# Kernel optimization log

Hardware: AMD Instinct MI355X
Metric: run time of the kernel (lower is better)

## Reference

```python
import jax, jax.numpy as jnp
import numpy as np

HIDDEN = 192
NDIM = 3
N_NODES = 262144
BATCH = 8
N_SUPER = 2048
DEG = 16
N_EDGES = BATCH * N_SUPER * DEG  # 262144
MAX_WAVELENGTH = 10000.0


def sincos_embed(coords):
    # ContinuousSincosEmbed: dim=192, ndim=3 -> 64 dims per coord (32 sin + 32 cos), no padding
    d_per = HIDDEN // NDIM  # 64
    omega = 1.0 / MAX_WAVELENGTH ** (jnp.arange(0, d_per, 2, dtype=jnp.float32) / d_per)  # [32]
    out = coords[:, :, None] * omega[None, None, :]            # [N, ndim, 32]
    emb = jnp.concatenate([jnp.sin(out), jnp.cos(out)], -1)    # [N, ndim, 64]
    return emb.reshape(coords.shape[0], HIDDEN)                # [N, 192]


def _xavier(key, fan_in, fan_out):
    bound = np.sqrt(6.0 / (fan_in + fan_out)).astype(np.float32)
    return jax.random.uniform(key, (fan_in, fan_out), jnp.float32, -bound, bound)


def setup_inputs() -> dict:
    key = jax.random.key(0)
    k = jax.random.split(key, 8)
    mesh_pos = jax.random.normal(k[0], (N_NODES, NDIM), jnp.float32)
    # edges grouped by sorted dst (segment_csr precondition); every supernode appears DEG times
    dst = jnp.repeat(jnp.arange(BATCH * N_SUPER, dtype=jnp.int32), DEG)          # [E]
    src = jax.random.randint(k[1], (N_EDGES,), 0, N_NODES, dtype=jnp.int32)      # [E]
    mesh_edges = jnp.stack([dst, src], axis=1)                                   # [E, 2]
    batch_idx = jnp.repeat(jnp.arange(BATCH, dtype=jnp.int32), N_NODES // BATCH)
    return {
        "mesh_pos": mesh_pos,
        "mesh_edges": mesh_edges,
        "batch_idx": batch_idx,
        "W1": _xavier(k[2], 2 * HIDDEN, 2 * HIDDEN), "b1": jnp.zeros((2 * HIDDEN,), jnp.float32),
        "W2": _xavier(k[3], 2 * HIDDEN, HIDDEN),     "b2": jnp.zeros((HIDDEN,), jnp.float32),
        "W3": _xavier(k[4], HIDDEN, HIDDEN),         "b3": jnp.zeros((HIDDEN,), jnp.float32),
    }


def reference(mesh_pos, mesh_edges, batch_idx, W1, b1, W2, b2, W3, b3):
    x = sincos_embed(mesh_pos)                       # [N, H]
    dst_idx = mesh_edges[:, 0]
    src_idx = mesh_edges[:, 1]
    h = jnp.concatenate([x[src_idx], x[dst_idx]], axis=1)        # [E, 2H]
    h = jax.nn.gelu(h @ W1 + b1, approximate=False)
    h = jax.nn.gelu(h @ W2 + b2, approximate=False)
    h = h @ W3 + b3                                              # [E, H]
    num_segments = BATCH * N_SUPER  # = number of unique dst by construction
    sums = jax.ops.segment_sum(h, dst_idx, num_segments=num_segments)
    counts = jax.ops.segment_sum(jnp.ones((h.shape[0],), h.dtype), dst_idx,
                                 num_segments=num_segments)
    mean = sums / jnp.maximum(counts, 1.0)[:, None]              # segment_csr mean
    return mean.reshape(BATCH, N_SUPER, HIDDEN)
```

## Files before the change

kernel.cpp:

```cpp
#include <hip/hip_runtime.h>

#define HID    192
#define HID2   384
#define NEDGES 262144
#define NSEG   16384
#define MB     64
#define NBLK   (NEDGES / MB)

#define ALD   200
#define H1LD  408
#define SMEM2 26112

typedef __bf16 bf16;
typedef __bf16 bv8 __attribute__((ext_vector_type(8)));
typedef __bf16 bv4 __attribute__((ext_vector_type(4)));
typedef float f32x4 __attribute__((ext_vector_type(4)));

__device__ __forceinline__ float gelu_fast(float x) {
    float x2 = x * x;
    float u2 = 1.5957691216057308f * x * __builtin_fmaf(0.044715f, x2, 1.0f);
    float e  = __expf(u2);
    float inv = __builtin_amdgcn_rcpf(e + 1.0f);
    return __builtin_fmaf(-x, inv, x);
}

__device__ __forceinline__ bv8 embed8(float p0, float p1, float p2, int t0) {
    const int dim   = t0 >> 6;
    const int isCos = t0 & 32;
    const int f0    = t0 & 31;
    const float pv  = (dim == 0) ? p0 : ((dim == 1) ? p1 : p2);
    float om = exp2f(-0.4152410118609203f * (float)f0);
    bv8 v;
    #pragma unroll
    for (int j = 0; j < 8; ++j) {
        const float x = pv * om;
        v[j] = (bf16)(isCos ? __cosf(x) : __sinf(x));
        om *= 0.74989420933245582f;
    }
    return v;
}

__global__ void wprep_kernel(const float* __restrict__ W1, const float* __restrict__ W2,
                             const float* __restrict__ W3,
                             bf16* __restrict__ W1T, bf16* __restrict__ W2T,
                             bf16* __restrict__ W3T) {
    __shared__ float t[32][33];
    int b = blockIdx.x;
    const float* S; bf16* D; int K, N, tk, tn;
    if (b < 144)      { S = W1; D = W1T; K = 384; N = 384; tk = (b / 12) * 32; tn = (b % 12) * 32; }
    else if (b < 216) { b -= 144; S = W2; D = W2T; K = 384; N = 192; tk = (b / 6) * 32; tn = (b % 6) * 32; }
    else              { b -= 216; S = W3; D = W3T; K = 192; N = 192; tk = (b / 6) * 32; tn = (b % 6) * 32; }
    const int c = threadIdx.x & 31, r0 = threadIdx.x >> 5;
    #pragma unroll
    for (int i = 0; i < 4; ++i)
        t[r0 + i * 8][c] = S[(size_t)(tk + r0 + i * 8) * N + tn + c];
    __syncthreads();
    #pragma unroll
    for (int i = 0; i < 4; ++i)
        D[(size_t)(tn + r0 + i * 8) * K + tk + c] = (bf16)t[c][r0 + i * 8];
}

__global__ __launch_bounds__(256, 3)
void dstc_kernel(const float* __restrict__ pos, const int* __restrict__ edges,
                 const bf16* __restrict__ W1T, bf16* __restrict__ dstC) {
    __shared__ __align__(16) bf16 smem[MB * ALD];
    const int tid = threadIdx.x, w = tid >> 6, lane = tid & 63;
    const int quad = lane >> 4, l15 = lane & 15, blk = blockIdx.x;
    {
        const int r = tid >> 2, part = tid & 3;
        const int node = edges[2 * ((blk * MB + r) * 16)];
        const float p0 = pos[node * 3 + 0], p1 = pos[node * 3 + 1], p2 = pos[node * 3 + 2];
        bf16* ldst = smem + r * ALD + part * 48;
        #pragma unroll
        for (int g = 0; g < 6; ++g)
            *reinterpret_cast<bv8*>(ldst + g * 8) = embed8(p0, p1, p2, part * 48 + g * 8);
    }
    __syncthreads();
    const f32x4 fz = {0.f, 0.f, 0.f, 0.f};
    f32x4 acc[6][4];
    #pragma unroll
    for (int mc = 0; mc < 6; ++mc)
        #pragma unroll
        for (int ne = 0; ne < 4; ++ne) acc[mc][ne] = fz;
    const bf16* wb = W1T + (size_t)(w * 96 + l15) * HID2 + 192 + quad * 8;
    const bf16* xb = smem + l15 * ALD + quad * 8;
    for (int kt = 0; kt < 6; ++kt) {
        bv8 x[4];
        #pragma unroll
        for (int ne = 0; ne < 4; ++ne)
            x[ne] = *reinterpret_cast<const bv8*>(xb + ne * 16 * ALD + kt * 32);
        #pragma unroll
        for (int mc = 0; mc < 6; ++mc) {
            bv8 a = *reinterpret_cast<const bv8*>(wb + mc * 16 * HID2 + kt * 32);
            #pragma unroll
            for (int ne = 0; ne < 4; ++ne)
                acc[mc][ne] = __builtin_amdgcn_mfma_f32_16x16x32_bf16(a, x[ne], acc[mc][ne], 0, 0, 0);
        }
    }
    #pragma unroll
    for (int mc = 0; mc < 6; ++mc)
        #pragma unroll
        for (int ne = 0; ne < 4; ++ne) {
            bv4 pk;
            #pragma unroll
            for (int r = 0; r < 4; ++r) pk[r] = (bf16)acc[mc][ne][r];
            *reinterpret_cast<bv4*>(dstC + (size_t)(blk * MB + ne * 16 + l15) * HID2
                                    + w * 96 + mc * 16 + quad * 4) = pk;
        }
}

__global__ __launch_bounds__(256, 3)
void fused_mlp_kernel(const float* __restrict__ pos, const int* __restrict__ edges,
                      const bf16* __restrict__ W1T, const float* __restrict__ b1,
                      const bf16* __restrict__ W2T, const float* __restrict__ b2,
                      const bf16* __restrict__ dstC, bf16* __restrict__ mh2) {
    __shared__ __align__(16) bf16 smem[SMEM2];
    const int tid = threadIdx.x, w = tid >> 6, lane = tid & 63;
    const int quad = lane >> 4, l15 = lane & 15, blk = blockIdx.x;

    {
        const int r = tid >> 2, part = tid & 3;
        const int node = edges[2 * (blk * MB + r) + 1];
        const float p0 = pos[node * 3 + 0], p1 = pos[node * 3 + 1], p2 = pos[node * 3 + 2];
        bf16* ldst = smem + r * ALD + part * 48;
        #pragma unroll
        for (int g = 0; g < 6; ++g)
            *reinterpret_cast<bv8*>(ldst + g * 8) = embed8(p0, p1, p2, part * 48 + g * 8);
    }
    __syncthreads();

    const f32x4 fz = {0.f, 0.f, 0.f, 0.f};

    f32x4 acc1[6][4];
    #pragma unroll
    for (int mc = 0; mc < 6; ++mc)
        #pragma unroll
        for (int ne = 0; ne < 4; ++ne) acc1[mc][ne] = fz;
    {
        const bf16* wb = W1T + (size_t)(w * 96 + l15) * HID2 + quad * 8;
        const bf16* xb = smem + l15 * ALD + quad * 8;
        for (int kt = 0; kt < 6; ++kt) {
            bv8 x[4];
            #pragma unroll
            for (int ne = 0; ne < 4; ++ne)
                x[ne] = *reinterpret_cast<const bv8*>(xb + ne * 16 * ALD + kt * 32);
            #pragma unroll
            for (int mc = 0; mc < 6; ++mc) {
                bv8 a = *reinterpret_cast<const bv8*>(wb + mc * 16 * HID2 + kt * 32);
                #pragma unroll
                for (int ne = 0; ne < 4; ++ne)
                    acc1[mc][ne] = __builtin_amdgcn_mfma_f32_16x16x32_bf16(a, x[ne], acc1[mc][ne], 0, 0, 0);
            }
        }
    }
    __syncthreads();

    {
        const int cb = w * 96 + quad * 4;
        #pragma unroll
        for (int mc = 0; mc < 6; ++mc) {
            f32x4 bia = *reinterpret_cast<const f32x4*>(b1 + cb + mc * 16);
            #pragma unroll
            for (int ne = 0; ne < 4; ++ne) {
                bv4 dc = *reinterpret_cast<const bv4*>(dstC + (size_t)(blk * 4 + ne) * HID2 + cb + mc * 16);
                bv4 o;
                #pragma unroll
                for (int r = 0; r < 4; ++r)
                    o[r] = (bf16)gelu_fast(acc1[mc][ne][r] + (float)dc[r] + bia[r]);
                *reinterpret_cast<bv4*>(smem + (ne * 16 + l15) * H1LD + cb + mc * 16) = o;
            }
        }
    }
    __syncthreads();

    f32x4 acc2[4][3];
    #pragma unroll
    for (int m = 0; m < 4; ++m)
        #pragma unroll
        for (int nc = 0; nc < 3; ++nc) acc2[m][nc] = fz;
    {
        const bf16* hb = smem + l15 * H1LD + quad * 8;
        const bf16* wb = W2T + (size_t)(w * 48 + l15) * HID2 + quad * 8;
        for (int kt = 0; kt < 12; ++kt) {
            bv8 h[4];
            #pragma unroll
            for (int m = 0; m < 4; ++m)
                h[m] = *reinterpret_cast<const bv8*>(hb + m * 16 * H1LD + kt * 32);
            #pragma unroll
            for (int nc = 0; nc < 3; ++nc) {
                bv8 b = *reinterpret_cast<const bv8*>(wb + nc * 16 * HID2 + kt * 32);
                #pragma unroll
                for (int m = 0; m < 4; ++m)
                    acc2[m][nc] = __builtin_amdgcn_mfma_f32_16x16x32_bf16(h[m], b, acc2[m][nc], 0, 0, 0);
            }
        }
    }

    #pragma unroll
    for (int nc = 0; nc < 3; ++nc) {
        const int colv = w * 48 + nc * 16 + l15;
        const float bia = b2[colv];
        #pragma unroll
        for (int m = 0; m < 4; ++m) {
            float s = gelu_fast(acc2[m][nc][0] + bia) + gelu_fast(acc2[m][nc][1] + bia)
                    + gelu_fast(acc2[m][nc][2] + bia) + gelu_fast(acc2[m][nc][3] + bia);
            s += __shfl_xor(s, 16);
            s += __shfl_xor(s, 32);
            if (quad == 0)
                mh2[(size_t)(blk * 4 + m) * HID + colv] = (bf16)(s * 0.0625f);
        }
    }
}

__global__ __launch_bounds__(256, 3)
void gemm3_kernel(const bf16* __restrict__ mh2, const bf16* __restrict__ W3T,
                  const float* __restrict__ b3, float* __restrict__ out) {
    __shared__ __align__(16) bf16 smem[128 * ALD];
    const int tid = threadIdx.x, w = tid >> 6, lane = tid & 63;
    const int quad = lane >> 4, l15 = lane & 15, blk = blockIdx.x;
    {
        const int r = tid >> 1, half = tid & 1;
        const bf16* src = mh2 + (size_t)(blk * 128 + r) * HID + half * 96;
        bf16* dst = smem + r * ALD + half * 96;
        #pragma unroll
        for (int i = 0; i < 12; ++i)
            reinterpret_cast<bv8*>(dst)[i] = reinterpret_cast<const bv8*>(src)[i];
    }
    __syncthreads();
    const f32x4 fz = {0.f, 0.f, 0.f, 0.f};
    f32x4 acc[8][3];
    #pragma unroll
    for (int mt = 0; mt < 8; ++mt)
        #pragma unroll
        for (int nc = 0; nc < 3; ++nc) acc[mt][nc] = fz;
    {
        const bf16* hb = smem + l15 * ALD + quad * 8;
        const bf16* wb = W3T + (size_t)(w * 48 + l15) * HID + quad * 8;
        for (int kt = 0; kt < 6; ++kt) {
            bv8 h[8];
            #pragma unroll
            for (int mt = 0; mt < 8; ++mt)
                h[mt] = *reinterpret_cast<const bv8*>(hb + mt * 16 * ALD + kt * 32);
            #pragma unroll
            for (int nc = 0; nc < 3; ++nc) {
                bv8 b = *reinterpret_cast<const bv8*>(wb + nc * 16 * HID + kt * 32);
                #pragma unroll
                for (int mt = 0; mt < 8; ++mt)
                    acc[mt][nc] = __builtin_amdgcn_mfma_f32_16x16x32_bf16(h[mt], b, acc[mt][nc], 0, 0, 0);
            }
        }
    }
    #pragma unroll
    for (int nc = 0; nc < 3; ++nc) {
        const int col = w * 48 + nc * 16 + l15;
        const float bia = b3[col];
        #pragma unroll
        for (int mt = 0; mt < 8; ++mt)
            #pragma unroll
            for (int r = 0; r < 4; ++r)
                out[(size_t)(blk * 128 + mt * 16 + quad * 4 + r) * HID + col] = acc[mt][nc][r] + bia;
    }
}

extern "C" void kernel_launch(void* const* d_in, const int* in_sizes, int n_in,
                              void* d_out, int out_size, void* d_ws, size_t ws_size,
                              hipStream_t stream) {
    const float* mesh_pos = (const float*)d_in[0];
    const int*   edges    = (const int*)  d_in[1];
    const float* W1 = (const float*)d_in[3];
    const float* b1 = (const float*)d_in[4];
    const float* W2 = (const float*)d_in[5];
    const float* b2 = (const float*)d_in[6];
    const float* W3 = (const float*)d_in[7];
    const float* b3 = (const float*)d_in[8];
    float* out = (float*)d_out;

    bf16* W1T  = (bf16*)d_ws;
    bf16* W2T  = W1T + 147456;
    bf16* W3T  = W2T + 73728;
    bf16* dstC = W3T + 36864;
    bf16* mh2  = dstC + (size_t)NSEG * HID2;

    wprep_kernel<<<252, 256, 0, stream>>>(W1, W2, W3, W1T, W2T, W3T);
    dstc_kernel<<<NSEG / MB, 256, 0, stream>>>(mesh_pos, edges, W1T, dstC);
    fused_mlp_kernel<<<NBLK, 256, 0, stream>>>(mesh_pos, edges, W1T, b1, W2T, b2, dstC, mh2);
    gemm3_kernel<<<NSEG / 128, 256, 0, stream>>>(mh2, W3T, b3, out);
}
```

Measured before the change: 274.9 us.

## Split fused MLP across 8 waves and keep separate LDS regions for stages

```diff
diff --git a/kernel.cpp b/kernel.cpp
--- a/kernel.cpp
+++ b/kernel.cpp
@@ -9,7 +9,8 @@
 
 #define ALD   200
 #define H1LD  408
-#define SMEM2 26112
+#define H1OFF 12800
+#define SMEM2 38912
 
 typedef __bf16 bf16;
 typedef __bf16 bv8 __attribute__((ext_vector_type(8)));
@@ -109,7 +110,7 @@
         }
 }
 
-__global__ __launch_bounds__(256, 3)
+__global__ __launch_bounds__(512, 4)
 void fused_mlp_kernel(const float* __restrict__ pos, const int* __restrict__ edges,
                       const bf16* __restrict__ W1T, const float* __restrict__ b1,
                       const bf16* __restrict__ W2T, const float* __restrict__ b2,
@@ -119,25 +120,25 @@
     const int quad = lane >> 4, l15 = lane & 15, blk = blockIdx.x;
 
     {
-        const int r = tid >> 2, part = tid & 3;
+        const int r = tid >> 3, part = tid & 7;
         const int node = edges[2 * (blk * MB + r) + 1];
         const float p0 = pos[node * 3 + 0], p1 = pos[node * 3 + 1], p2 = pos[node * 3 + 2];
-        bf16* ldst = smem + r * ALD + part * 48;
-        #pragma unroll
-        for (int g = 0; g < 6; ++g)
-            *reinterpret_cast<bv8*>(ldst + g * 8) = embed8(p0, p1, p2, part * 48 + g * 8);
+        bf16* ldst = smem + r * ALD + part * 24;
+        #pragma unroll
+        for (int g = 0; g < 3; ++g)
+            *reinterpret_cast<bv8*>(ldst + g * 8) = embed8(p0, p1, p2, part * 24 + g * 8);
     }
     __syncthreads();
 
     const f32x4 fz = {0.f, 0.f, 0.f, 0.f};
 
-    f32x4 acc1[6][4];
-    #pragma unroll
-    for (int mc = 0; mc < 6; ++mc)
+    f32x4 acc1[3][4];
+    #pragma unroll
+    for (int mc = 0; mc < 3; ++mc)
         #pragma unroll
         for (int ne = 0; ne < 4; ++ne) acc1[mc][ne] = fz;
     {
-        const bf16* wb = W1T + (size_t)(w * 96 + l15) * HID2 + quad * 8;
+        const bf16* wb = W1T + (size_t)(w * 48 + l15) * HID2 + quad * 8;
         const bf16* xb = smem + l15 * ALD + quad * 8;
         for (int kt = 0; kt < 6; ++kt) {
             bv8 x[4];
@@ -145,7 +146,7 @@
             for (int ne = 0; ne < 4; ++ne)
                 x[ne] = *reinterpret_cast<const bv8*>(xb + ne * 16 * ALD + kt * 32);
             #pragma unroll
-            for (int mc = 0; mc < 6; ++mc) {
+            for (int mc = 0; mc < 3; ++mc) {
                 bv8 a = *reinterpret_cast<const bv8*>(wb + mc * 16 * HID2 + kt * 32);
                 #pragma unroll
                 for (int ne = 0; ne < 4; ++ne)
@@ -153,61 +154,71 @@
             }
         }
     }
-    __syncthreads();
-
-    {
-        const int cb = w * 96 + quad * 4;
-        #pragma unroll
-        for (int mc = 0; mc < 6; ++mc) {
-            f32x4 bia = *reinterpret_cast<const f32x4*>(b1 + cb + mc * 16);
+
+    {
+        #pragma unroll
+        for (int mc = 0; mc < 3; ++mc) {
+            const int cb = w * 48 + mc * 16 + quad * 4;
+            f32x4 bia = *reinterpret_cast<const f32x4*>(b1 + cb);
             #pragma unroll
             for (int ne = 0; ne < 4; ++ne) {
-                bv4 dc = *reinterpret_cast<const bv4*>(dstC + (size_t)(blk * 4 + ne) * HID2 + cb + mc * 16);
+                bv4 dc = *reinterpret_cast<const bv4*>(dstC + (size_t)(blk * 4 + ne) * HID2 + cb);
                 bv4 o;
                 #pragma unroll
                 for (int r = 0; r < 4; ++r)
                     o[r] = (bf16)gelu_fast(acc1[mc][ne][r] + (float)dc[r] + bia[r]);
-                *reinterpret_cast<bv4*>(smem + (ne * 16 + l15) * H1LD + cb + mc * 16) = o;
-            }
-        }
-    }
-    __syncthreads();
-
-    f32x4 acc2[4][3];
-    #pragma unroll
-    for (int m = 0; m < 4; ++m)
-        #pragma unroll
-        for (int nc = 0; nc < 3; ++nc) acc2[m][nc] = fz;
-    {
-        const bf16* hb = smem + l15 * H1LD + quad * 8;
-        const bf16* wb = W2T + (size_t)(w * 48 + l15) * HID2 + quad * 8;
+                *reinterpret_cast<bv4*>(smem + H1OFF + (ne * 16 + l15) * H1LD + cb) = o;
+            }
+        }
+    }
+    __syncthreads();
+
+    const int cg = w & 3, eg = w >> 2;
+    f32x4 acc2[3][2];
+    #pragma unroll
+    for (int mc = 0; mc < 3; ++mc)
+        #pragma unroll
+        for (int ne = 0; ne < 2; ++ne) acc2[mc][ne] = fz;
+    {
+        const bf16* wb = W2T + (size_t)(cg * 48 + l15) * HID2 + quad * 8;
+        const bf16* hb = smem + H1OFF + (eg * 32 + l15) * H1LD + quad * 8;
         for (int kt = 0; kt < 12; ++kt) {
-            bv8 h[4];
-            #pragma unroll
-            for (int m = 0; m < 4; ++m)
-                h[m] = *reinterpret_cast<const bv8*>(hb + m * 16 * H1LD + kt * 32);
-            #pragma unroll
-            for (int nc = 0; nc < 3; ++nc) {
-                bv8 b = *reinterpret_cast<const bv8*>(wb + nc * 16 * HID2 + kt * 32);
-                #pragma unroll
-                for (int m = 0; m < 4; ++m)
-                    acc2[m][nc] = __builtin_amdgcn_mfma_f32_16x16x32_bf16(h[m], b, acc2[m][nc], 0, 0, 0);
-            }
-        }
-    }
-
-    #pragma unroll
-    for (int nc = 0; nc < 3; ++nc) {
-        const int colv = w * 48 + nc * 16 + l15;
-        const float bia = b2[colv];
-        #pragma unroll
-        for (int m = 0; m < 4; ++m) {
-            float s = gelu_fast(acc2[m][nc][0] + bia) + gelu_fast(acc2[m][nc][1] + bia)
-                    + gelu_fast(acc2[m][nc][2] + bia) + gelu_fast(acc2[m][nc][3] + bia);
-            s += __shfl_xor(s, 16);
-            s += __shfl_xor(s, 32);
-            if (quad == 0)
-                mh2[(size_t)(blk * 4 + m) * HID + colv] = (bf16)(s * 0.0625f);
+            bv8 h[2];
+            #pragma unroll
+            for (int ne = 0; ne < 2; ++ne)
+                h[ne] = *reinterpret_cast<const bv8*>(hb + ne * 16 * H1LD + kt * 32);
+            #pragma unroll
+            for (int mc = 0; mc < 3; ++mc) {
+                bv8 a = *reinterpret_cast<const bv8*>(wb + mc * 16 * HID2 + kt * 32);
+                #pragma unroll
+                for (int ne = 0; ne < 2; ++ne)
+                    acc2[mc][ne] = __builtin_amdgcn_mfma_f32_16x16x32_bf16(a, h[ne], acc2[mc][ne], 0, 0, 0);
+            }
+        }
+    }
+
+    #pragma unroll
+    for (int mc = 0; mc < 3; ++mc) {
+        const int cb = cg * 48 + mc * 16 + quad * 4;
+        f32x4 bia = *reinterpret_cast<const f32x4*>(b2 + cb);
+        #pragma unroll
+        for (int ne = 0; ne < 2; ++ne) {
+            float s[4];
+            #pragma unroll
+            for (int r = 0; r < 4; ++r) {
+                float v = gelu_fast(acc2[mc][ne][r] + bia[r]);
+                v += __shfl_xor(v, 1);
+                v += __shfl_xor(v, 2);
+                v += __shfl_xor(v, 4);
+                v += __shfl_xor(v, 8);
+                s[r] = v;
+            }
+            if (l15 == 0) {
+                bv4 pk;
+                #pragma unroll
+                for (int r = 0; r < 4; ++r) pk[r] = (bf16)(s[r] * 0.0625f);
+                *reinterpret_cast<bv4*>(mh2 + (size_t)(blk * 4 + eg * 2 + ne) * HID + cb) = pk;
+            }
         }
     }
 }
@@ -283,6 +294,6 @@
 
     wprep_kernel<<<252, 256, 0, stream>>>(W1, W2, W3, W1T, W2T, W3T);
     dstc_kernel<<<NSEG / MB, 256, 0, stream>>>(mesh_pos, edges, W1T, dstC);
-    fused_mlp_kernel<<<NBLK, 256, 0, stream>>>(mesh_pos, edges, W1T, b1, W2T, b2, dstC, mh2);
+    fused_mlp_kernel<<<NBLK, 512, 0, stream>>>(mesh_pos, edges, W1T, b1, W2T, b2, dstC, mh2);
     gemm3_kernel<<<NSEG / 128, 256, 0, stream>>>(mh2, W3T, b3, out);
 }
```

Measured after the change: 346.7 us. 1.26x slower.

## Merge weight prep with dst projection and fuse final GEMM into MLP kernel

Applied to the files above, without the earlier changes.

```diff
diff --git a/kernel.cpp b/kernel.cpp
--- a/kernel.cpp
+++ b/kernel.cpp
@@ -9,7 +9,8 @@
 
 #define ALD   200
 #define H1LD  408
-#define SMEM2 26112
+#define MH2   26112
+#define SMEM2 26880
 
 typedef __bf16 bf16;
 typedef __bf16 bv8 __attribute__((ext_vector_type(8)));
@@ -40,32 +41,33 @@
     return v;
 }
 
-__global__ void wprep_kernel(const float* __restrict__ W1, const float* __restrict__ W2,
-                             const float* __restrict__ W3,
-                             bf16* __restrict__ W1T, bf16* __restrict__ W2T,
-                             bf16* __restrict__ W3T) {
-    __shared__ float t[32][33];
-    int b = blockIdx.x;
-    const float* S; bf16* D; int K, N, tk, tn;
-    if (b < 144)      { S = W1; D = W1T; K = 384; N = 384; tk = (b / 12) * 32; tn = (b % 12) * 32; }
-    else if (b < 216) { b -= 144; S = W2; D = W2T; K = 384; N = 192; tk = (b / 6) * 32; tn = (b % 6) * 32; }
-    else              { b -= 216; S = W3; D = W3T; K = 192; N = 192; tk = (b / 6) * 32; tn = (b % 6) * 32; }
-    const int c = threadIdx.x & 31, r0 = threadIdx.x >> 5;
-    #pragma unroll
-    for (int i = 0; i < 4; ++i)
-        t[r0 + i * 8][c] = S[(size_t)(tk + r0 + i * 8) * N + tn + c];
-    __syncthreads();
-    #pragma unroll
-    for (int i = 0; i < 4; ++i)
-        D[(size_t)(tn + r0 + i * 8) * K + tk + c] = (bf16)t[c][r0 + i * 8];
-}
-
-__global__ __launch_bounds__(256, 3)
-void dstc_kernel(const float* __restrict__ pos, const int* __restrict__ edges,
-                 const bf16* __restrict__ W1T, bf16* __restrict__ dstC) {
+__global__ __launch_bounds__(256)
+void prep_kernel(const float* __restrict__ W1, const float* __restrict__ W2,
+                 const float* __restrict__ W3,
+                 const float* __restrict__ pos, const int* __restrict__ edges,
+                 bf16* __restrict__ W1T, bf16* __restrict__ W2T, bf16* __restrict__ W3T,
+                 bf16* __restrict__ dstC) {
+    if (blockIdx.x < 252) {
+        __shared__ float t[32][33];
+        int b = blockIdx.x;
+        const float* S; bf16* D; int K, N, tk, tn;
+        if (b < 144)      { S = W1; D = W1T; K = 384; N = 384; tk = (b / 12) * 32; tn = (b % 12) * 32; }
+        else if (b < 216) { b -= 144; S = W2; D = W2T; K = 384; N = 192; tk = (b / 6) * 32; tn = (b % 6) * 32; }
+        else              { b -= 216; S = W3; D = W3T; K = 192; N = 192; tk = (b / 6) * 32; tn = (b % 6) * 32; }
+        const int c = threadIdx.x & 31, r0 = threadIdx.x >> 5;
+        #pragma unroll
+        for (int i = 0; i < 4; ++i)
+            t[r0 + i * 8][c] = S[(size_t)(tk + r0 + i * 8) * N + tn + c];
+        __syncthreads();
+        #pragma unroll
+        for (int i = 0; i < 4; ++i)
+            D[(size_t)(tn + r0 + i * 8) * K + tk + c] = (bf16)t[c][r0 + i * 8];
+        return;
+    }
     __shared__ __align__(16) bf16 smem[MB * ALD];
     const int tid = threadIdx.x, w = tid >> 6, lane = tid & 63;
-    const int quad = lane >> 4, l15 = lane & 15, blk = blockIdx.x;
+    const int quad = lane >> 4, l15 = lane & 15;
+    const int blk = blockIdx.x - 252;
     {
         const int r = tid >> 2, part = tid & 3;
         const int node = edges[2 * ((blk * MB + r) * 16)];
@@ -82,7 +84,6 @@
     for (int mc = 0; mc < 6; ++mc)
         #pragma unroll
         for (int ne = 0; ne < 4; ++ne) acc[mc][ne] = fz;
-    const bf16* wb = W1T + (size_t)(w * 96 + l15) * HID2 + 192 + quad * 8;
     const bf16* xb = smem + l15 * ALD + quad * 8;
     for (int kt = 0; kt < 6; ++kt) {
         bv8 x[4];
@@ -91,7 +92,11 @@
             x[ne] = *reinterpret_cast<const bv8*>(xb + ne * 16 * ALD + kt * 32);
         #pragma unroll
         for (int mc = 0; mc < 6; ++mc) {
-            bv8 a = *reinterpret_cast<const bv8*>(wb + mc * 16 * HID2 + kt * 32);
+            bv8 a;
+            const int col = w * 96 + mc * 16 + l15;
+            #pragma unroll
+            for (int j = 0; j < 8; ++j)
+                a[j] = (bf16)W1[(size_t)(192 + kt * 32 + quad * 8 + j) * HID2 + col];
             #pragma unroll
             for (int ne = 0; ne < 4; ++ne)
                 acc[mc][ne] = __builtin_amdgcn_mfma_f32_16x16x32_bf16(a, x[ne], acc[mc][ne], 0, 0, 0);
@@ -113,7 +118,8 @@
 void fused_mlp_kernel(const float* __restrict__ pos, const int* __restrict__ edges,
                       const bf16* __restrict__ W1T, const float* __restrict__ b1,
                       const bf16* __restrict__ W2T, const float* __restrict__ b2,
-                      const bf16* __restrict__ dstC, bf16* __restrict__ mh2) {
+                      const bf16* __restrict__ W3T, const float* __restrict__ b3,
+                      const bf16* __restrict__ dstC, float* __restrict__ out) {
     __shared__ __align__(16) bf16 smem[SMEM2];
     const int tid = threadIdx.x, w = tid >> 6, lane = tid & 63;
     const int quad = lane >> 4, l15 = lane & 15, blk = blockIdx.x;
@@ -156,18 +162,18 @@
     __syncthreads();
 
     {
-        const int cb = w * 96 + quad * 4;
         #pragma unroll
         for (int mc = 0; mc < 6; ++mc) {
-            f32x4 bia = *reinterpret_cast<const f32x4*>(b1 + cb + mc * 16);
+            const int cb = w * 96 + mc * 16 + quad * 4;
+            f32x4 bia = *reinterpret_cast<const f32x4*>(b1 + cb);
             #pragma unroll
             for (int ne = 0; ne < 4; ++ne) {
-                bv4 dc = *reinterpret_cast<const bv4*>(dstC + (size_t)(blk * 4 + ne) * HID2 + cb + mc * 16);
+                bv4 dc = *reinterpret_cast<const bv4*>(dstC + (size_t)(blk * 4 + ne) * HID2 + cb);
                 bv4 o;
                 #pragma unroll
                 for (int r = 0; r < 4; ++r)
                     o[r] = (bf16)gelu_fast(acc1[mc][ne][r] + (float)dc[r] + bia[r]);
-                *reinterpret_cast<bv4*>(smem + (ne * 16 + l15) * H1LD + cb + mc * 16) = o;
+                *reinterpret_cast<bv4*>(smem + (ne * 16 + l15) * H1LD + cb) = o;
             }
         }
     }
@@ -207,58 +213,35 @@
             s += __shfl_xor(s, 16);
             s += __shfl_xor(s, 32);
             if (quad == 0)
-                mh2[(size_t)(blk * 4 + m) * HID + colv] = (bf16)(s * 0.0625f);
-        }
-    }
-}
-
-__global__ __launch_bounds__(256, 3)
-void gemm3_kernel(const bf16* __restrict__ mh2, const bf16* __restrict__ W3T,
-                  const float* __restrict__ b3, float* __restrict__ out) {
-    __shared__ __align__(16) bf16 smem[128 * ALD];
-    const int tid = threadIdx.x, w = tid >> 6, lane = tid & 63;
-    const int quad = lane >> 4, l15 = lane & 15, blk = blockIdx.x;
-    {
-        const int r = tid >> 1, half = tid & 1;
-        const bf16* src = mh2 + (size_t)(blk * 128 + r) * HID + half * 96;
-        bf16* dst = smem + r * ALD + half * 96;
-        #pragma unroll
-        for (int i = 0; i < 12; ++i)
-            reinterpret_cast<bv8*>(dst)[i] = reinterpret_cast<const bv8*>(src)[i];
-    }
-    __syncthreads();
-    const f32x4 fz = {0.f, 0.f, 0.f, 0.f};
-    f32x4 acc[8][3];
-    #pragma unroll
-    for (int mt = 0; mt < 8; ++mt)
-        #pragma unroll
-        for (int nc = 0; nc < 3; ++nc) acc[mt][nc] = fz;
-    {
-        const bf16* hb = smem + l15 * ALD + quad * 8;
+                smem[MH2 + m * HID + colv] = (bf16)(s * 0.0625f);
+        }
+    }
+    __syncthreads();
+
+    {
+        f32x4 acc3[3];
+        #pragma unroll
+        for (int nc = 0; nc < 3; ++nc) acc3[nc] = fz;
+        const bf16* ab = smem + MH2 + (l15 & 3) * HID + quad * 8;
         const bf16* wb = W3T + (size_t)(w * 48 + l15) * HID + quad * 8;
         for (int kt = 0; kt < 6; ++kt) {
-            bv8 h[8];
-            #pragma unroll
-            for (int mt = 0; mt < 8; ++mt)
-                h[mt] = *reinterpret_cast<const bv8*>(hb + mt * 16 * ALD + kt * 32);
+            bv8 a = *reinterpret_cast<const bv8*>(ab + kt * 32);
             #pragma unroll
             for (int nc = 0; nc < 3; ++nc) {
                 bv8 b = *reinterpret_cast<const bv8*>(wb + nc * 16 * HID + kt * 32);
-                #pragma unroll
-                for (int mt = 0; mt < 8; ++mt)
-                    acc[mt][nc] = __builtin_amdgcn_mfma_f32_16x16x32_bf16(h[mt], b, acc[mt][nc], 0, 0, 0);
-            }
-        }
-    }
-    #pragma unroll
-    for (int nc = 0; nc < 3; ++nc) {
-        const int col = w * 48 + nc * 16 + l15;
-        const float bia = b3[col];
-        #pragma unroll
-        for (int mt = 0; mt < 8; ++mt)
-            #pragma unroll
-            for (int r = 0; r < 4; ++r)
-                out[(size_t)(blk * 128 + mt * 16 + quad * 4 + r) * HID + col] = acc[mt][nc][r] + bia;
+                acc3[nc] = __builtin_amdgcn_mfma_f32_16x16x32_bf16(a, b, acc3[nc], 0, 0, 0);
+            }
+        }
+        if (quad == 0) {
+            #pragma unroll
+            for (int nc = 0; nc < 3; ++nc) {
+                const int col   = w * 48 + nc * 16 + l15;
+                const float bia = b3[col];
+                #pragma unroll
+                for (int r = 0; r < 4; ++r)
+                    out[(size_t)(blk * 4 + r) * HID + col] = acc3[nc][r] + bia;
+            }
+        }
     }
 }
 
@@ -279,10 +262,8 @@
     bf16* W2T  = W1T + 147456;
     bf16* W3T  = W2T + 73728;
     bf16* dstC = W3T + 36864;
-    bf16* mh2  = dstC + (size_t)NSEG * HID2;
-
-    wprep_kernel<<<252, 256, 0, stream>>>(W1, W2, W3, W1T, W2T, W3T);
-    dstc_kernel<<<NSEG / MB, 256, 0, stream>>>(mesh_pos, edges, W1T, dstC);
-    fused_mlp_kernel<<<NBLK, 256, 0, stream>>>(mesh_pos, edges, W1T, b1, W2T, b2, dstC, mh2);
-    gemm3_kernel<<<NSEG / 128, 256, 0, stream>>>(mh2, W3T, b3, out);
-}
+
+    prep_kernel<<<508, 256, 0, stream>>>(W1, W2, W3, mesh_pos, edges, W1T, W2T, W3T, dstC);
+    fused_mlp_kernel<<<NBLK, 256, 0, stream>>>(mesh_pos, edges, W1T, b1, W2T, b2, W3T, b3,
+                                               dstC, out);
+}
```

Result: no change. 276.8 us (+0.7%).
